# Optimization experiments

Measured on AMD Instinct MI355X. Metric: run time of the kernel, lower is better.

The kernel has to match this reference:

```python
import jax, jax.numpy as jnp
import numpy as np

IN, H, T = 16, 64, 25

def _lstm_layer(x, w_ih, w_hh, b_ih, b_hh):
    # x: [B,T,I]; w_ih: [4H,I]; w_hh: [4H,H]; biases: [4H]
    B = x.shape[0]
    x_proj = jnp.einsum('bti,gi->btg', x, w_ih) + b_ih + b_hh  # [B,T,4H]
    h0 = jnp.zeros((B, H), x.dtype)
    c0 = jnp.zeros((B, H), x.dtype)
    def step(carry, xt):
        h, c = carry
        gates = xt + h @ w_hh.T  # [B,4H]
        i, f, g, o = jnp.split(gates, 4, axis=-1)  # torch gate order i,f,g,o
        i = jax.nn.sigmoid(i); f = jax.nn.sigmoid(f)
        g = jnp.tanh(g);       o = jax.nn.sigmoid(o)
        c = f * c + i * g
        h = o * jnp.tanh(c)
        return (h, c), h
    _, hs = jax.lax.scan(step, (h0, c0), jnp.swapaxes(x_proj, 0, 1))  # [T,B,H]
    return jnp.swapaxes(hs, 0, 1)  # [B,T,H]


def setup_inputs() -> dict:
    key = jax.random.key(0)
    ks = jax.random.split(key, 20)
    s = 1.0 / np.sqrt(H)
    u = lambda k, shp: jax.random.uniform(k, shp, jnp.float32, -s, s)
    inp = {
        'x': jax.random.normal(ks[0], (32768, T, IN), jnp.float32),
        'w_ih0': u(ks[1], (4 * H, IN)), 'w_hh0': u(ks[2], (4 * H, H)),
        'b_ih0': u(ks[3], (4 * H,)),    'b_hh0': u(ks[4], (4 * H,)),
        'w_ih1': u(ks[5], (4 * H, H)),  'w_hh1': u(ks[6], (4 * H, H)),
        'b_ih1': u(ks[7], (4 * H,)),    'b_hh1': u(ks[8], (4 * H,)),
        'fc1_w': u(ks[9],  (128, H * T)), 'fc1_b': u(ks[10], (128,)),
        'fc2_w': u(ks[11], (128, H * T)), 'fc2_b': u(ks[12], (128,)),
        'fc3_w': u(ks[13], (128, H * T)), 'fc3_b': u(ks[14], (128,)),
        'l1_w': u(ks[15], (5, 128)),  'l1_b': u(ks[16], (5,)),
        'l2_w': u(ks[17], (4, 128)),  'l2_b': u(ks[18], (4,)),
        'l3_w': u(ks[19], (8, 128)),  'l3_b': jnp.zeros((8,), jnp.float32),
    }
    return inp


def reference(x, w_ih0, w_hh0, b_ih0, b_hh0, w_ih1, w_hh1, b_ih1, b_hh1,
              fc1_w, fc1_b, fc2_w, fc2_b, fc3_w, fc3_b,
              l1_w, l1_b, l2_w, l2_b, l3_w, l3_b):
    out = _lstm_layer(x, w_ih0, w_hh0, b_ih0, b_hh0)
    out = _lstm_layer(out, w_ih1, w_hh1, b_ih1, b_hh1)  # [B,T,H]
    flat = out.reshape(out.shape[0], -1)  # [B, T*H]
    x1 = jax.nn.relu(flat @ fc1_w.T + fc1_b)
    x2 = jax.nn.relu(flat @ fc2_w.T + fc2_b)
    x3 = jax.nn.relu(flat @ fc3_w.T + fc3_b)
    o1 = x1 @ l1_w.T + l1_b
    o2 = x2 @ l2_w.T + l2_b
    o3 = x3 @ l3_w.T + l3_b
    return (o1, o2, o3)
```

## Files before the change

kernel.cpp:

```cpp
#include <hip/hip_runtime.h>
#include <stdint.h>

#define BATCH 32768
#define TT    25

typedef float f32x4 __attribute__((ext_vector_type(4)));
typedef short s16x8 __attribute__((ext_vector_type(8)));

__device__ __align__(16) short g_Wc[384 * 1600];

#define LOG2E 1.442695040888963f

__device__ __forceinline__ uint32_t f2bf(float v){
  uint32_t u = __float_as_uint(v);
  return (u + 0x7fffu + ((u >> 16) & 1u)) >> 16;
}
__device__ __forceinline__ short f2bfs(float v){ return (short)f2bf(v); }

__device__ __forceinline__ uint32_t cvt_pk_bf16(float lo, float hi){
  uint32_t d;
  asm("v_cvt_pk_bf16_f32 %0, %1, %2" : "=v"(d) : "v"(lo), "v"(hi));
  return d;
}

__device__ __forceinline__ float sigm(float x){
  float e = __builtin_amdgcn_exp2f(-LOG2E * x);
  return __builtin_amdgcn_rcpf(1.0f + e);
}
__device__ __forceinline__ float tanh_(float x){
  float e = __builtin_amdgcn_exp2f(-2.0f*LOG2E * x);
  return 2.0f*__builtin_amdgcn_rcpf(1.0f + e) - 1.0f;
}
__device__ __forceinline__ s16x8 pack8(float4 a, float4 b){
  s16x8 v;
  v[0]=f2bfs(a.x); v[1]=f2bfs(a.y); v[2]=f2bfs(a.z); v[3]=f2bfs(a.w);
  v[4]=f2bfs(b.x); v[5]=f2bfs(b.y); v[6]=f2bfs(b.z); v[7]=f2bfs(b.w);
  return v;
}

__global__ void conv_wc_kernel(const float* __restrict__ fc1w,
                               const float* __restrict__ fc2w,
                               const float* __restrict__ fc3w){
  const int j = blockIdx.x;
  const float* src = (j < 128) ? fc1w + j*1600
                   : (j < 256) ? fc2w + (j-128)*1600
                               : fc3w + (j-256)*1600;
  for (int k = threadIdx.x; k < 1600; k += 256)
    g_Wc[j*1600 + k] = f2bfs(src[k]);
}

__global__ __launch_bounds__(512, 1) void lstm2_mfma_kernel(
    const float* __restrict__ x,
    const float* __restrict__ wih0, const float* __restrict__ whh0,
    const float* __restrict__ bih0, const float* __restrict__ bhh0,
    const float* __restrict__ wih1, const float* __restrict__ whh1,
    const float* __restrict__ bih1, const float* __restrict__ bhh1,
    short* __restrict__ flat)
{
  __shared__ short Abuf[4*64*64];
  char* const Ab = (char*)Abuf;

  const int tid  = threadIdx.x;
  const int lane = tid & 63;
  const int wv   = tid >> 6;
  const int w4   = wv & 3;
  const int wg   = wv >> 2;
  const int lrow = lane & 15;
  const int lk   = lane >> 4;
  const int sw   = (lrow & 7) << 4;
  const int sb   = blockIdx.x * 64;
  const int u    = w4*16 + lrow;

  {
    s16x8 z = {0,0,0,0,0,0,0,0};
    int idx = tid * 32;
    char* pz = Ab + ((idx < 8192) ? 8192 + idx : 16384 + idx);
    *(s16x8*)pz = z; *(s16x8*)(pz + 16) = z;
  }

  s16x8 W1f[4][4], B0x[4], B0h[4][2];
  #pragma unroll
  for (int n = 0; n < 4; n++){
    const int g = n*64 + u;
    #pragma unroll
    for (int kt = 0; kt < 4; kt++){
      const float* src = (kt < 2 ? wih1 + g*64 + kt*32 : whh1 + g*64 + (kt-2)*32) + lk*8;
      W1f[n][kt] = pack8(*(const float4*)src, *(const float4*)(src+4));
    }
    if (lk < 2){
      const float* src = wih0 + g*16 + lk*8;
      B0x[n] = pack8(*(const float4*)src, *(const float4*)(src+4));
    } else {
      s16x8 z = {0,0,0,0,0,0,0,0}; B0x[n] = z;
    }
    #pragma unroll
    for (int kt = 0; kt < 2; kt++){
      const float* src = whh0 + g*64 + kt*32 + lk*8;
      B0h[n][kt] = pack8(*(const float4*)src, *(const float4*)(src+4));
    }
  }

  float b0v[4], b1v[4];
  #pragma unroll
  for (int n = 0; n < 4; n++){
    b0v[n] = bih0[n*64+u] + bhh0[n*64+u];
    b1v[n] = bih1[n*64+u] + bhh1[n*64+u];
  }

  const float* xbase[2];
  #pragma unroll
  for (int m = 0; m < 2; m++)
    xbase[m] = x + (size_t)(sb + wg*32 + m*16 + lrow)*(TT*16) + (lk&1)*8;
  s16x8 xf[2];
  #pragma unroll
  for (int m = 0; m < 2; m++)
    xf[m] = pack8(*(const float4*)(xbase[m]), *(const float4*)(xbase[m] + 4));

  float c0[2][4], c1[2][4];
  #pragma unroll
  for (int m = 0; m < 2; m++)
    #pragma unroll
    for (int r = 0; r < 4; r++){ c0[m][r] = 0.f; c1[m][r] = 0.f; }

  __syncthreads();

  #pragma unroll 1
  for (int t = 0; t < TT; t++){
    const int p  = t & 1;
    const int pn = p ^ 1;
    f32x4 acc[2][4];
    #pragma unroll
    for (int m = 0; m < 2; m++)
      #pragma unroll
      for (int n = 0; n < 4; n++){ f32x4 iv = {b0v[n],b0v[n],b0v[n],b0v[n]}; acc[m][n] = iv; }
    #pragma unroll
    for (int m = 0; m < 2; m++)
      #pragma unroll
      for (int n = 0; n < 4; n++)
        acc[m][n] = __builtin_amdgcn_mfma_f32_16x16x32_bf16(xf[m], B0x[n], acc[m][n], 0, 0, 0);
    #pragma unroll
    for (int kt = 0; kt < 2; kt++){
      s16x8 a[2];
      #pragma unroll
      for (int m = 0; m < 2; m++){
        int row = wg*32 + m*16 + lrow;
        a[m] = *(const s16x8*)(Ab + pn*8192 + row*128 + ((kt*64 + lk*16) ^ sw));
      }
      #pragma unroll
      for (int m = 0; m < 2; m++)
        #pragma unroll
        for (int n = 0; n < 4; n++)
          acc[m][n] = __builtin_amdgcn_mfma_f32_16x16x32_bf16(a[m], B0h[n][kt], acc[m][n], 0, 0, 0);
    }
    short hb[2][4];
    #pragma unroll
    for (int m = 0; m < 2; m++)
      #pragma unroll
      for (int r = 0; r < 4; r++){
        float iv = sigm(acc[m][0][r]);
        float fv = sigm(acc[m][1][r]);
        float gv = tanh_(acc[m][2][r]);
        float ov = sigm(acc[m][3][r]);
        float c  = fmaf(fv, c0[m][r], iv*gv); c0[m][r] = c;
        hb[m][r] = f2bfs(ov * tanh_(c));
      }
    #pragma unroll
    for (int m = 0; m < 2; m++)
      #pragma unroll
      for (int r = 0; r < 4; r++){
        int mine = (int)(uint16_t)hb[m][r];
        int part = __shfl_xor(mine, 1);
        if ((lane & 1) == 0){
          int s_ = wg*32 + m*16 + lk*4 + r;
          uint32_t pk = (uint32_t)mine | ((uint32_t)part << 16);
          *(uint32_t*)(Ab + p*8192 + s_*128 + ((u*2) ^ ((s_&7)<<4))) = pk;
        }
      }
    __syncthreads();

    s16x8 xfn[2];
    if (t + 1 < TT){
      #pragma unroll
      for (int m = 0; m < 2; m++)
        xfn[m] = pack8(*(const float4*)(xbase[m] + (t+1)*16),
                       *(const float4*)(xbase[m] + (t+1)*16 + 4));
    }
    #pragma unroll
    for (int m = 0; m < 2; m++)
      #pragma unroll
      for (int n = 0; n < 4; n++){ f32x4 iv = {b1v[n],b1v[n],b1v[n],b1v[n]}; acc[m][n] = iv; }
    #pragma unroll
    for (int kt = 0; kt < 4; kt++){
      const int reg = (kt < 2) ? p*8192 : 16384 + pn*8192;
      const int ko  = (kt & 1) * 64;
      s16x8 a[2];
      #pragma unroll
      for (int m = 0; m < 2; m++){
        int row = wg*32 + m*16 + lrow;
        a[m] = *(const s16x8*)(Ab + reg + row*128 + ((ko + lk*16) ^ sw));
      }
      #pragma unroll
      for (int m = 0; m < 2; m++)
        #pragma unroll
        for (int n = 0; n < 4; n++)
          acc[m][n] = __builtin_amdgcn_mfma_f32_16x16x32_bf16(a[m], W1f[n][kt], acc[m][n], 0, 0, 0);
    }
    #pragma unroll
    for (int m = 0; m < 2; m++)
      #pragma unroll
      for (int r = 0; r < 4; r++){
        float iv = sigm(acc[m][0][r]);
        float fv = sigm(acc[m][1][r]);
        float gv = tanh_(acc[m][2][r]);
        float ov = sigm(acc[m][3][r]);
        float c  = fmaf(fv, c1[m][r], iv*gv); c1[m][r] = c;
        hb[m][r] = f2bfs(ov * tanh_(c));
      }
    #pragma unroll
    for (int m = 0; m < 2; m++)
      #pragma unroll
      for (int r = 0; r < 4; r++){
        int mine = (int)(uint16_t)hb[m][r];
        int part = __shfl_xor(mine, 1);
        if ((lane & 1) == 0){
          int s_ = wg*32 + m*16 + lk*4 + r;
          uint32_t pk = (uint32_t)mine | ((uint32_t)part << 16);
          *(uint32_t*)(Ab + 16384 + p*8192 + s_*128 + ((u*2) ^ ((s_&7)<<4))) = pk;
          *(uint32_t*)(flat + (size_t)(sb+s_)*1600 + t*64 + u) = pk;
        }
      }
    #pragma unroll
    for (int m = 0; m < 2; m++) xf[m] = xfn[m];
  }
}

__global__ __launch_bounds__(256,1) void fc_mfma_kernel(
    const short* __restrict__ flat,
    const float* __restrict__ fc1b, const float* __restrict__ fc2b, const float* __restrict__ fc3b,
    const float* __restrict__ l1w,  const float* __restrict__ l1b,
    const float* __restrict__ l2w,  const float* __restrict__ l2b,
    const float* __restrict__ l3w,  const float* __restrict__ l3b,
    float* __restrict__ out)
{
  __shared__ short Rs[64*384];
  char* const Rb = (char*)Rs;
  const int tid  = threadIdx.x;
  const int lane = tid & 63;
  const int wv   = tid >> 6;
  const int lrow = lane & 15;
  const int lk   = lane >> 4;
  const int sb   = blockIdx.x * 64;

  f32x4 acc[4][6];
  #pragma unroll
  for (int n = 0; n < 6; n++){
    int j = wv*96 + n*16 + lrow;
    float bv = (j < 128) ? fc1b[j] : (j < 256) ? fc2b[j-128] : fc3b[j-256];
    #pragma unroll
    for (int m = 0; m < 4; m++){ f32x4 iv = {bv,bv,bv,bv}; acc[m][n] = iv; }
  }

  const char* Abase = (const char*)(flat + (size_t)sb*1600);
  const char* Bbase = (const char*)g_Wc;
  #pragma unroll 1
  for (int kc = 0; kc < 50; kc++){
    s16x8 a[4], b[6];
    #pragma unroll
    for (int m = 0; m < 4; m++)
      a[m] = *(const s16x8*)(Abase + (size_t)(m*16+lrow)*3200 + kc*64 + lk*16);
    #pragma unroll
    for (int n = 0; n < 6; n++)
      b[n] = *(const s16x8*)(Bbase + (size_t)(wv*96+n*16+lrow)*3200 + kc*64 + lk*16);
    #pragma unroll
    for (int m = 0; m < 4; m++)
      #pragma unroll
      for (int n = 0; n < 6; n++)
        acc[m][n] = __builtin_amdgcn_mfma_f32_16x16x32_bf16(a[m], b[n], acc[m][n], 0, 0, 0);
  }

  #pragma unroll
  for (int m = 0; m < 4; m++)
    #pragma unroll
    for (int n = 0; n < 6; n++)
      #pragma unroll
      for (int r = 0; r < 4; r++){
        float v  = fmaxf(acc[m][n][r], 0.f);
        float vp = __shfl_xor(v, 1);
        uint32_t pk = cvt_pk_bf16(v, vp);
        if ((lane & 1) == 0){
          int s_ = m*16 + lk*4 + r;
          int fc = wv*96 + n*16 + lrow;
          *(uint32_t*)(Rb + s_*768 + ((fc*2) ^ ((s_&7)<<4))) = pk;
        }
      }
  __syncthreads();

  const float* Lw[3] = {l1w, l2w, l3w};
  const int   odim[3] = {5, 4, 8};
  s16x8 Bh[3][4];
  #pragma unroll
  for (int q = 0; q < 3; q++){
    #pragma unroll
    for (int kt = 0; kt < 4; kt++){
      if (lrow < odim[q]){
        const float* src = Lw[q] + lrow*128 + kt*32 + lk*8;
        Bh[q][kt] = pack8(*(const float4*)src, *(const float4*)(src+4));
      } else {
        s16x8 z = {0,0,0,0,0,0,0,0}; Bh[q][kt] = z;
      }
    }
  }
  f32x4 acc2[4][3];
  {
    float bv0 = (lrow < 5) ? l1b[lrow] : 0.f;
    float bv1 = (lrow < 4) ? l2b[lrow] : 0.f;
    float bv2 = (lrow < 8) ? l3b[lrow] : 0.f;
    #pragma unroll
    for (int m = 0; m < 4; m++){
      f32x4 i0 = {bv0,bv0,bv0,bv0}; acc2[m][0] = i0;
      f32x4 i1 = {bv1,bv1,bv1,bv1}; acc2[m][1] = i1;
      f32x4 i2 = {bv2,bv2,bv2,bv2}; acc2[m][2] = i2;
    }
  }
  #pragma unroll
  for (int q = 0; q < 3; q++){
    #pragma unroll
    for (int kt = 0; kt < 4; kt++){
      s16x8 a[4];
      #pragma unroll
      for (int m = 0; m < 4; m++){
        int row = m*16 + lrow;
        a[m] = *(const s16x8*)(Rb + row*768 + ((q*256 + kt*64 + lk*16) ^ ((row&7)<<4)));
      }
      #pragma unroll
      for (int m = 0; m < 4; m++)
        acc2[m][q] = __builtin_amdgcn_mfma_f32_16x16x32_bf16(a[m], Bh[q][kt], acc2[m][q], 0, 0, 0);
    }
  }
  #pragma unroll
  for (int m = 0; m < 4; m++)
    #pragma unroll
    for (int r = 0; r < 4; r++){
      int smp = sb + m*16 + lk*4 + r;
      if (lrow < 5) out[(size_t)smp*5 + lrow] = acc2[m][0][r];
      if (lrow < 4) out[(size_t)BATCH*5 + (size_t)smp*4 + lrow] = acc2[m][1][r];
      if (lrow < 8) out[(size_t)BATCH*9 + (size_t)smp*8 + lrow] = acc2[m][2][r];
    }
}

extern "C" void kernel_launch(void* const* d_in, const int* in_sizes, int n_in,
                              void* d_out, int out_size, void* d_ws, size_t ws_size,
                              hipStream_t stream)
{
  const float* x    = (const float*)d_in[0];
  const float* wih0 = (const float*)d_in[1];
  const float* whh0 = (const float*)d_in[2];
  const float* bih0 = (const float*)d_in[3];
  const float* bhh0 = (const float*)d_in[4];
  const float* wih1 = (const float*)d_in[5];
  const float* whh1 = (const float*)d_in[6];
  const float* bih1 = (const float*)d_in[7];
  const float* bhh1 = (const float*)d_in[8];
  const float* fc1w = (const float*)d_in[9];
  const float* fc1b = (const float*)d_in[10];
  const float* fc2w = (const float*)d_in[11];
  const float* fc2b = (const float*)d_in[12];
  const float* fc3w = (const float*)d_in[13];
  const float* fc3b = (const float*)d_in[14];
  const float* l1w  = (const float*)d_in[15];
  const float* l1b  = (const float*)d_in[16];
  const float* l2w  = (const float*)d_in[17];
  const float* l2b  = (const float*)d_in[18];
  const float* l3w  = (const float*)d_in[19];
  const float* l3b  = (const float*)d_in[20];

  float* out  = (float*)d_out;
  short* flat = (short*)d_ws;
  if (ws_size < (size_t)BATCH*1600*2) return;

  conv_wc_kernel<<<dim3(384), dim3(256), 0, stream>>>(fc1w, fc2w, fc3w);

  lstm2_mfma_kernel<<<dim3(BATCH/64), dim3(512), 0, stream>>>(
      x, wih0, whh0, bih0, bhh0, wih1, whh1, bih1, bhh1, flat);

  fc_mfma_kernel<<<dim3(BATCH/64), dim3(256), 0, stream>>>(
      flat, fc1b, fc2b, fc3b, l1w, l1b, l2w, l2b, l3w, l3b, out);
}
```

Baseline: 375.2 us.

## Double FC kernel waves, split head work per wave, use cheaper bf16 rounding

The FC kernel now launches 512 threads per block, so each of 8 waves computes 48 output columns instead of 96. The small head GEMMs are split so six waves each handle one head and half the rows, instead of every wave redundantly computing all heads. The LSTM kernel swaps round-to-nearest-even bf16 conversion for a cheaper round-half-up on x and hidden states, which cuts ALU work in the recurrent loop but changes rounding slightly. More waves raise latency hiding in the FC loop, at the cost of each wave reloading the shared A fragments.

```diff
diff --git a/kernel.cpp b/kernel.cpp
--- a/kernel.cpp
+++ b/kernel.cpp
@@ -17,10 +17,8 @@
 }
 __device__ __forceinline__ short f2bfs(float v){ return (short)f2bf(v); }
 
-__device__ __forceinline__ uint32_t cvt_pk_bf16(float lo, float hi){
-  uint32_t d;
-  asm("v_cvt_pk_bf16_f32 %0, %1, %2" : "=v"(d) : "v"(lo), "v"(hi));
-  return d;
+__device__ __forceinline__ short f2bfs_fast(float v){
+  return (short)((__float_as_uint(v) + 0x8000u) >> 16);
 }
 
 __device__ __forceinline__ float sigm(float x){
@@ -35,6 +33,12 @@
   s16x8 v;
   v[0]=f2bfs(a.x); v[1]=f2bfs(a.y); v[2]=f2bfs(a.z); v[3]=f2bfs(a.w);
   v[4]=f2bfs(b.x); v[5]=f2bfs(b.y); v[6]=f2bfs(b.z); v[7]=f2bfs(b.w);
+  return v;
+}
+__device__ __forceinline__ s16x8 pack8_fast(float4 a, float4 b){
+  s16x8 v;
+  v[0]=f2bfs_fast(a.x); v[1]=f2bfs_fast(a.y); v[2]=f2bfs_fast(a.z); v[3]=f2bfs_fast(a.w);
+  v[4]=f2bfs_fast(b.x); v[5]=f2bfs_fast(b.y); v[6]=f2bfs_fast(b.z); v[7]=f2bfs_fast(b.w);
   return v;
 }
 
@@ -114,7 +118,7 @@
   s16x8 xf[2];
   #pragma unroll
   for (int m = 0; m < 2; m++)
-    xf[m] = pack8(*(const float4*)(xbase[m]), *(const float4*)(xbase[m] + 4));
+    xf[m] = pack8_fast(*(const float4*)(xbase[m]), *(const float4*)(xbase[m] + 4));
 
   float c0[2][4], c1[2][4];
   #pragma unroll
@@ -162,7 +166,7 @@
         float gv = tanh_(acc[m][2][r]);
         float ov = sigm(acc[m][3][r]);
         float c  = fmaf(fv, c0[m][r], iv*gv); c0[m][r] = c;
-        hb[m][r] = f2bfs(ov * tanh_(c));
+        hb[m][r] = f2bfs_fast(ov * tanh_(c));
       }
     #pragma unroll
     for (int m = 0; m < 2; m++)
@@ -182,8 +186,8 @@
     if (t + 1 < TT){
       #pragma unroll
       for (int m = 0; m < 2; m++)
-        xfn[m] = pack8(*(const float4*)(xbase[m] + (t+1)*16),
-                       *(const float4*)(xbase[m] + (t+1)*16 + 4));
+        xfn[m] = pack8_fast(*(const float4*)(xbase[m] + (t+1)*16),
+                            *(const float4*)(xbase[m] + (t+1)*16 + 4));
     }
     #pragma unroll
     for (int m = 0; m < 2; m++)
@@ -214,7 +218,7 @@
         float gv = tanh_(acc[m][2][r]);
         float ov = sigm(acc[m][3][r]);
         float c  = fmaf(fv, c1[m][r], iv*gv); c1[m][r] = c;
-        hb[m][r] = f2bfs(ov * tanh_(c));
+        hb[m][r] = f2bfs_fast(ov * tanh_(c));
       }
     #pragma unroll
     for (int m = 0; m < 2; m++)
@@ -234,7 +238,7 @@
   }
 }
 
-__global__ __launch_bounds__(256,1) void fc_mfma_kernel(
+__global__ __launch_bounds__(512,1) void fc_mfma_kernel(
     const short* __restrict__ flat,
     const float* __restrict__ fc1b, const float* __restrict__ fc2b, const float* __restrict__ fc3b,
     const float* __restrict__ l1w,  const float* __restrict__ l1b,
@@ -251,10 +255,10 @@
   const int lk   = lane >> 4;
   const int sb   = blockIdx.x * 64;
 
-  f32x4 acc[4][6];
-  #pragma unroll
-  for (int n = 0; n < 6; n++){
-    int j = wv*96 + n*16 + lrow;
+  f32x4 acc[4][3];
+  #pragma unroll
+  for (int n = 0; n < 3; n++){
+    int j = wv*48 + n*16 + lrow;
     float bv = (j < 128) ? fc1b[j] : (j < 256) ? fc2b[j-128] : fc3b[j-256];
     #pragma unroll
     for (int m = 0; m < 4; m++){ f32x4 iv = {bv,bv,bv,bv}; acc[m][n] = iv; }
@@ -264,88 +268,84 @@
   const char* Bbase = (const char*)g_Wc;
   #pragma unroll 1
   for (int kc = 0; kc < 50; kc++){
-    s16x8 a[4], b[6];
+    s16x8 a[4], b[3];
     #pragma unroll
     for (int m = 0; m < 4; m++)
       a[m] = *(const s16x8*)(Abase + (size_t)(m*16+lrow)*3200 + kc*64 + lk*16);
     #pragma unroll
-    for (int n = 0; n < 6; n++)
-      b[n] = *(const s16x8*)(Bbase + (size_t)(wv*96+n*16+lrow)*3200 + kc*64 + lk*16);
+    for (int n = 0; n < 3; n++)
+      b[n] = *(const s16x8*)(Bbase + (size_t)(wv*48+n*16+lrow)*3200 + kc*64 + lk*16);
     #pragma unroll
     for (int m = 0; m < 4; m++)
       #pragma unroll
-      for (int n = 0; n < 6; n++)
+      for (int n = 0; n < 3; n++)
         acc[m][n] = __builtin_amdgcn_mfma_f32_16x16x32_bf16(a[m], b[n], acc[m][n], 0, 0, 0);
   }
 
   #pragma unroll
   for (int m = 0; m < 4; m++)
     #pragma unroll
-    for (int n = 0; n < 6; n++)
+    for (int n = 0; n < 3; n++)
       #pragma unroll
       for (int r = 0; r < 4; r++){
         float v  = fmaxf(acc[m][n][r], 0.f);
         float vp = __shfl_xor(v, 1);
-        uint32_t pk = cvt_pk_bf16(v, vp);
         if ((lane & 1) == 0){
           int s_ = m*16 + lk*4 + r;
-          int fc = wv*96 + n*16 + lrow;
+          int fc = wv*48 + n*16 + lrow;
+          uint32_t pk = (uint32_t)(uint16_t)f2bfs_fast(v)
+                      | ((uint32_t)(uint16_t)f2bfs_fast(vp) << 16);
           *(uint32_t*)(Rb + s_*768 + ((fc*2) ^ ((s_&7)<<4))) = pk;
         }
       }
   __syncthreads();
 
-  const float* Lw[3] = {l1w, l2w, l3w};
-  const int   odim[3] = {5, 4, 8};
-  s16x8 Bh[3][4];
-  #pragma unroll
-  for (int q = 0; q < 3; q++){
+  if (wv < 6){
+    const int q  = wv >> 1;
+    const int mh = wv & 1;
+    const float* Lw  = (q==0) ? l1w : (q==1) ? l2w : l3w;
+    const float* Lb  = (q==0) ? l1b : (q==1) ? l2b : l3b;
+    const int odim   = (q==0) ? 5 : (q==1) ? 4 : 8;
+    s16x8 Bh[4];
     #pragma unroll
     for (int kt = 0; kt < 4; kt++){
-      if (lrow < odim[q]){
-        const float* src = Lw[q] + lrow*128 + kt*32 + lk*8;
-        Bh[q][kt] = pack8(*(const float4*)src, *(const float4*)(src+4));
+      if (lrow < odim){
+        const float* src = Lw + lrow*128 + kt*32 + lk*8;
+        Bh[kt] = pack8(*(const float4*)src, *(const float4*)(src+4));
       } else {
-        s16x8 z = {0,0,0,0,0,0,0,0}; Bh[q][kt] = z;
-      }
-    }
-  }
-  f32x4 acc2[4][3];
-  {
-    float bv0 = (lrow < 5) ? l1b[lrow] : 0.f;
-    float bv1 = (lrow < 4) ? l2b[lrow] : 0.f;
-    float bv2 = (lrow < 8) ? l3b[lrow] : 0.f;
-    #pragma unroll
-    for (int m = 0; m < 4; m++){
-      f32x4 i0 = {bv0,bv0,bv0,bv0}; acc2[m][0] = i0;
-      f32x4 i1 = {bv1,bv1,bv1,bv1}; acc2[m][1] = i1;
-      f32x4 i2 = {bv2,bv2,bv2,bv2}; acc2[m][2] = i2;
-    }
-  }
-  #pragma unroll
-  for (int q = 0; q < 3; q++){
+        s16x8 z = {0,0,0,0,0,0,0,0}; Bh[kt] = z;
+      }
+    }
+    float bv = (lrow < odim) ? Lb[lrow] : 0.f;
+    f32x4 acc2[2];
+    #pragma unroll
+    for (int mm = 0; mm < 2; mm++){ f32x4 iv = {bv,bv,bv,bv}; acc2[mm] = iv; }
     #pragma unroll
     for (int kt = 0; kt < 4; kt++){
-      s16x8 a[4];
-      #pragma unroll
-      for (int m = 0; m < 4; m++){
-        int row = m*16 + lrow;
-        a[m] = *(const s16x8*)(Rb + row*768 + ((q*256 + kt*64 + lk*16) ^ ((row&7)<<4)));
-      }
-      #pragma unroll
-      for (int m = 0; m < 4; m++)
-        acc2[m][q] = __builtin_amdgcn_mfma_f32_16x16x32_bf16(a[m], Bh[q][kt], acc2[m][q], 0, 0, 0);
-    }
-  }
-  #pragma unroll
-  for (int m = 0; m < 4; m++)
-    #pragma unroll
-    for (int r = 0; r < 4; r++){
-      int smp = sb + m*16 + lk*4 + r;
-      if (lrow < 5) out[(size_t)smp*5 + lrow] = acc2[m][0][r];
-      if (lrow < 4) out[(size_t)BATCH*5 + (size_t)smp*4 + lrow] = acc2[m][1][r];
-      if (lrow < 8) out[(size_t)BATCH*9 + (size_t)smp*8 + lrow] = acc2[m][2][r];
-    }
+      s16x8 av[2];
+      #pragma unroll
+      for (int mm = 0; mm < 2; mm++){
+        int row = (mh*2+mm)*16 + lrow;
+        av[mm] = *(const s16x8*)(Rb + row*768 + ((q*256 + kt*64 + lk*16) ^ ((row&7)<<4)));
+      }
+      #pragma unroll
+      for (int mm = 0; mm < 2; mm++)
+        acc2[mm] = __builtin_amdgcn_mfma_f32_16x16x32_bf16(av[mm], Bh[kt], acc2[mm], 0, 0, 0);
+    }
+    #pragma unroll
+    for (int mm = 0; mm < 2; mm++)
+      #pragma unroll
+      for (int r = 0; r < 4; r++){
+        int smp = sb + (mh*2+mm)*16 + lk*4 + r;
+        if (q == 0){
+          if (lrow < 5) out[(size_t)smp*5 + lrow] = acc2[mm][r];
+        } else if (q == 1){
+          if (lrow < 4) out[(size_t)BATCH*5 + (size_t)smp*4 + lrow] = acc2[mm][r];
+        } else {
+          if (lrow < 8) out[(size_t)BATCH*9 + (size_t)smp*8 + lrow] = acc2[mm][r];
+        }
+      }
+  }
 }
 
 extern "C" void kernel_launch(void* const* d_in, const int* in_sizes, int n_in,
@@ -383,6 +383,6 @@
   lstm2_mfma_kernel<<<dim3(BATCH/64), dim3(512), 0, stream>>>(
       x, wih0, whh0, bih0, bhh0, wih1, whh1, bih1, bhh1, flat);
 
-  fc_mfma_kernel<<<dim3(BATCH/64), dim3(256), 0, stream>>>(
+  fc_mfma_kernel<<<dim3(BATCH/64), dim3(512), 0, stream>>>(
       flat, fc1b, fc2b, fc3b, l1w, l1b, l2w, l2b, l3w, l3b, out);
 }
```

Result: slower. 417.3 us (+11.2%).
